# Performance work log

Hardware: AMD Instinct MI355X
Metric: run time of the kernel (lower is better)

The kernel has to match this reference:

```python
import jax, jax.numpy as jnp
import numpy as np

B, T, H, I, E = 2, 2048, 1024, 2048, 8
TOP_K = 2
RMS_EPS = 1e-6
ROUTING_GAIN = 1.0
INIT_STD = 0.02


def setup_inputs() -> dict:
    key = jax.random.key(0)
    ks = jax.random.split(key, 6)
    x = jax.random.normal(ks[0], (B, T, H), dtype=jnp.float32)
    q_norm_w = jnp.ones((H,), dtype=jnp.float32)
    k_proto = jax.random.normal(ks[1], (E, H), dtype=jnp.float32) * INIT_STD
    v_proto = jnp.eye(E, dtype=jnp.float32)  # nn.init.eye_
    gate_projs = jax.random.normal(ks[2], (E, H, I), dtype=jnp.float32) * INIT_STD
    up_projs = jax.random.normal(ks[3], (E, H, I), dtype=jnp.float32) * INIT_STD
    down_projs = jax.random.normal(ks[4], (E, I, H), dtype=jnp.float32) * INIT_STD
    return {"x": x, "q_norm_w": q_norm_w, "k_proto": k_proto, "v_proto": v_proto,
            "gate_projs": gate_projs, "up_projs": up_projs, "down_projs": down_projs}


def _routing_weights(x, q_norm_w, k_proto, v_proto):
    # CAPRRouter: RMSNorm -> proto attention -> softmax -> value mix -> gain
    q = x * jax.lax.rsqrt(jnp.mean(x * x, axis=-1, keepdims=True) + RMS_EPS) * q_norm_w
    attn = jax.nn.softmax(jnp.einsum('bth,ph->btp', q, k_proto) / np.sqrt(H).astype(np.float32), axis=-1)
    logits = jnp.einsum('btp,pq->btq', attn, v_proto) * ROUTING_GAIN
    rw = jax.nn.softmax(logits, axis=-1)  # [B,T,E]
    if TOP_K < E:
        tw, ti = jax.lax.top_k(rw, TOP_K)                       # [B,T,k]
        onehot = jax.nn.one_hot(ti, E, dtype=rw.dtype)          # [B,T,k,E]
        rw = jnp.einsum('btk,btke->bte', tw, onehot)            # scatter top-k back
        rw = rw / (jnp.sum(rw, axis=-1, keepdims=True) + 1e-9)
    return rw


def reference(x, q_norm_w, k_proto, v_proto, gate_projs, up_projs, down_projs):
    rw = _routing_weights(x, q_norm_w, k_proto, v_proto)  # [B,T,E]
    # Math-equivalent reassociation of torch's ('btp,phi->bthi' then 'bth,bthi->bti'):
    # per-expert GEMM then routing-weighted reduction over experts.
    gate_out = jnp.einsum('btp,btpi->bti', rw, jnp.einsum('bth,phi->btpi', x, gate_projs))
    up_out = jnp.einsum('btp,btpi->bti', rw, jnp.einsum('bth,phi->btpi', x, up_projs))
    intermediate = jax.nn.silu(gate_out) * up_out  # [B,T,I]
    output = jnp.einsum('btp,btph->bth', rw, jnp.einsum('bti,pih->btph', intermediate, down_projs))
    return output, rw
```

## Files before the change

kernel.cpp:

```cpp
#include <hip/hip_runtime.h>
#include <hip/hip_bf16.h>

#define NTOK 4096
#define HDIM 1024
#define IDIM 2048
#define NEXP 8
#define RBLK 16

typedef __attribute__((ext_vector_type(8))) short short8;
typedef __attribute__((ext_vector_type(4))) short short4b;
typedef __attribute__((ext_vector_type(4))) float f32x4;
typedef unsigned short ushort_t;

__device__ inline ushort_t f2bf(float f) {
    union { float f; unsigned u; } v; v.f = f;
    unsigned r = v.u + 0x7FFFu + ((v.u >> 16) & 1u);
    return (ushort_t)(r >> 16);
}
__device__ inline float bf2f(ushort_t h) {
    union { unsigned u; float f; } v; v.u = ((unsigned)h) << 16;
    return v.f;
}

#define GPTR(p) ((const __attribute__((address_space(1))) void*)(p))
#define LPTR(p) ((__attribute__((address_space(3))) void*)(p))

__global__ __launch_bounds__(256) void routing_kernel(
    const float* __restrict__ x, const float* __restrict__ qw,
    const float* __restrict__ kp, const float* __restrict__ vp,
    float* __restrict__ rw_out, int* __restrict__ counts,
    int* __restrict__ list, float2* __restrict__ topw,
    ushort_t* __restrict__ xb)
{
    __shared__ float kp_s[NEXP * HDIM];
    __shared__ float vp_s[NEXP * NEXP];
    __shared__ int lcnt[NEXP];
    __shared__ int base_s[NEXP];
    __shared__ int tinfo[RBLK][4];

    int tid = threadIdx.x;
    int wid = tid >> 6, lane = tid & 63;

    if (tid < NEXP) lcnt[tid] = 0;
    if (tid < NEXP * NEXP) vp_s[tid] = vp[tid];
    #pragma unroll
    for (int i = 0; i < 8; i++)
        ((float4*)kp_s)[tid + 256 * i] = ((const float4*)kp)[tid + 256 * i];

    float4 qv[4];
    #pragma unroll
    for (int j = 0; j < 4; j++) qv[j] = ((const float4*)qw)[lane + 64 * j];
    __syncthreads();

    for (int it = 0; it < RBLK / 4; it++) {
        int tl = wid * (RBLK / 4) + it;
        int t = blockIdx.x * RBLK + tl;
        const float4* xr4 = (const float4*)(x + (size_t)t * HDIM);
        float4 xv[4];
        #pragma unroll
        for (int j = 0; j < 4; j++) xv[j] = xr4[lane + 64 * j];

        ushort_t* xrow = xb + (size_t)t * HDIM;
        #pragma unroll
        for (int j = 0; j < 4; j++) {
            short4b o;
            o[0] = f2bf(xv[j].x); o[1] = f2bf(xv[j].y);
            o[2] = f2bf(xv[j].z); o[3] = f2bf(xv[j].w);
            ((short4b*)xrow)[lane + 64 * j] = o;
        }

        float ss = 0.f;
        #pragma unroll
        for (int j = 0; j < 4; j++)
            ss += xv[j].x*xv[j].x + xv[j].y*xv[j].y + xv[j].z*xv[j].z + xv[j].w*xv[j].w;
        #pragma unroll
        for (int off = 32; off; off >>= 1) ss += __shfl_xor(ss, off);
        float rms = rsqrtf(ss * (1.0f / HDIM) + 1e-6f);

        float4 q[4];
        #pragma unroll
        for (int j = 0; j < 4; j++) {
            q[j].x = xv[j].x * rms * qv[j].x; q[j].y = xv[j].y * rms * qv[j].y;
            q[j].z = xv[j].z * rms * qv[j].z; q[j].w = xv[j].w * rms * qv[j].w;
        }

        float d[NEXP];
        #pragma unroll
        for (int p = 0; p < NEXP; p++) {
            float acc = 0.f;
            #pragma unroll
            for (int j = 0; j < 4; j++) {
                float4 kv = ((const float4*)kp_s)[p * 256 + lane + 64 * j];
                acc += q[j].x*kv.x + q[j].y*kv.y + q[j].z*kv.z + q[j].w*kv.w;
            }
            #pragma unroll
            for (int off = 32; off; off >>= 1) acc += __shfl_xor(acc, off);
            d[p] = acc * (1.0f / 32.0f);
        }

        float m = d[0];
        #pragma unroll
        for (int p = 1; p < NEXP; p++) m = fmaxf(m, d[p]);
        float a[NEXP]; float s = 0.f;
        #pragma unroll
        for (int p = 0; p < NEXP; p++) { a[p] = expf(d[p] - m); s += a[p]; }
        float inv = 1.0f / s;
        #pragma unroll
        for (int p = 0; p < NEXP; p++) a[p] *= inv;
        float lg[NEXP];
        #pragma unroll
        for (int qi = 0; qi < NEXP; qi++) {
            float acc = 0.f;
            #pragma unroll
            for (int p = 0; p < NEXP; p++) acc += a[p] * vp_s[p * NEXP + qi];
            lg[qi] = acc;
        }
        float m2 = lg[0];
        #pragma unroll
        for (int p = 1; p < NEXP; p++) m2 = fmaxf(m2, lg[p]);
        float r[NEXP]; float s2 = 0.f;
        #pragma unroll
        for (int p = 0; p < NEXP; p++) { r[p] = expf(lg[p] - m2); s2 += r[p]; }
        float inv2 = 1.0f / s2;
        #pragma unroll
        for (int p = 0; p < NEXP; p++) r[p] *= inv2;
        int e0 = -1, e1 = -1; float w0 = -1.f, w1 = -1.f;
        #pragma unroll
        for (int p = 0; p < NEXP; p++) {
            if (r[p] > w0) { w1 = w0; e1 = e0; w0 = r[p]; e0 = p; }
            else if (r[p] > w1) { w1 = r[p]; e1 = p; }
        }
        float invn = 1.0f / (w0 + w1 + 1e-9f);
        float w0n = w0 * invn, w1n = w1 * invn;

        if (lane == 0) {
            #pragma unroll
            for (int p = 0; p < NEXP; p++)
                rw_out[(size_t)t * NEXP + p] = (p == e0) ? w0n : ((p == e1) ? w1n : 0.f);
            topw[t] = make_float2(w0n, w1n);
            int p0 = atomicAdd(&lcnt[e0], 1);
            int p1 = atomicAdd(&lcnt[e1], 1);
            tinfo[tl][0] = e0; tinfo[tl][1] = p0;
            tinfo[tl][2] = e1; tinfo[tl][3] = p1;
        }
    }
    __syncthreads();
    if (tid < NEXP) base_s[tid] = atomicAdd(&counts[tid], lcnt[tid]);
    __syncthreads();
    if (tid < RBLK) {
        int t = blockIdx.x * RBLK + tid;
        int e0 = tinfo[tid][0], p0 = tinfo[tid][1];
        int e1 = tinfo[tid][2], p1 = tinfo[tid][3];
        list[e0 * NTOK + base_s[e0] + p0] = t * 2;
        list[e1 * NTOK + base_s[e1] + p1] = t * 2 + 1;
    }
}

__global__ __launch_bounds__(256) void conv_t(const float* __restrict__ in, ushort_t* __restrict__ out,
                                              int K, int N) {
    __shared__ ushort_t ts[64][72];
    int e = blockIdx.z;
    int xb = blockIdx.x, yb = blockIdx.y;
    const float* ip = in + (size_t)e * K * N + (size_t)(yb * 64) * N + xb * 64;
    int NB = N / 128, KB = K / 64;
    int nb = xb >> 1, rhalf = (xb & 1) * 64;
    ushort_t* op = out + ((size_t)((size_t)e * NB + nb) * KB + yb) * (128 * 64);

    int tid = threadIdx.x;
    int r0 = tid >> 4;
    int c4 = (tid & 15) * 4;
    #pragma unroll
    for (int i = 0; i < 4; i++) {
        int r = r0 + i * 16;
        float4 v = *(const float4*)(ip + (size_t)r * N + c4);
        ts[c4+0][r] = f2bf(v.x); ts[c4+1][r] = f2bf(v.y);
        ts[c4+2][r] = f2bf(v.z); ts[c4+3][r] = f2bf(v.w);
    }
    __syncthreads();
    int n = tid >> 2;
    int kq = (tid & 3) * 16;
    int sw = (n & 7) << 3;
    short8 w0 = *(const short8*)&ts[n][kq];
    short8 w1 = *(const short8*)&ts[n][kq + 8];
    ushort_t* dst = op + (size_t)(rhalf + n) * 64;
    *(short8*)(dst + (kq ^ sw))       = w0;
    *(short8*)(dst + ((kq + 8) ^ sw)) = w1;
}

template<int K, int FUSED>
__global__ __launch_bounds__(256) void gemm_bf16(
    const ushort_t* __restrict__ A,
    const ushort_t* __restrict__ W0, const ushort_t* __restrict__ W1,
    const int* __restrict__ counts, const int* __restrict__ list,
    ushort_t* __restrict__ out0, ushort_t* __restrict__ out1, int odim)
{
    constexpr int KB = K / 64;
    int e = blockIdx.z;
    int M = counts[e];
    int row0 = blockIdx.y * 128;
    if (row0 >= M) return;
    int nbTiles = odim / 128;
    int colb = blockIdx.x;
    const ushort_t* W = (FUSED && colb >= nbTiles) ? W1 : W0;
    ushort_t* outp    = (FUSED && colb >= nbTiles) ? out1 : out0;
    int nb = (FUSED && colb >= nbTiles) ? colb - nbTiles : colb;
    int col0 = nb * 128;

    __shared__ ushort_t smem[128 * 136];
    __shared__ int rowsS[128];
    ushort_t* Abuf = smem;
    ushort_t* Bbuf = smem + 8192;

    int tid = threadIdx.x;
    if (tid < 128) {
        int r = row0 + tid;
        rowsS[tid] = (r < M) ? list[e * NTOK + r] : -1;
    }
    __syncthreads();

    int wid = tid >> 6, lane = tid & 63;
    int wr = wid >> 1, wc = wid & 1;
    int la = lane & 15, lb = lane >> 4;

    int swu = (((lane & 7) ^ (lane >> 3)) * 8);
    const ushort_t* aP[4];
    #pragma unroll
    for (int i = 0; i < 4; i++) {
        int r = (wid * 4 + i) * 8 + (lane >> 3);
        int ent = rowsS[r];
        int tok = (ent >= 0) ? (ent >> 1) : 0;
        aP[i] = A + (size_t)tok * K + swu;
    }
    const ushort_t* Wt = W + (size_t)((size_t)e * nbTiles + nb) * ((size_t)KB * 8192);

    int swr = (la & 7) << 3;
    int aoff[4][2], boff[4][2];
    #pragma unroll
    for (int m = 0; m < 4; m++)
        #pragma unroll
        for (int ks = 0; ks < 2; ks++)
            aoff[m][ks] = (wr * 64 + m * 16 + la) * 64 + ((ks * 32 + lb * 8) ^ swr);
    #pragma unroll
    for (int n = 0; n < 4; n++)
        #pragma unroll
        for (int ks = 0; ks < 2; ks++)
            boff[n][ks] = (wc * 64 + n * 16 + la) * 64 + ((ks * 32 + lb * 8) ^ swr);

    f32x4 acc[4][4];
    #pragma unroll
    for (int m = 0; m < 4; m++)
        #pragma unroll
        for (int n = 0; n < 4; n++) acc[m][n] = (f32x4){0.f, 0.f, 0.f, 0.f};

    for (int kt = 0; kt < KB; kt++) {
        #pragma unroll
        for (int i = 0; i < 4; i++) {
            int seg = wid * 4 + i;
            __builtin_amdgcn_global_load_lds(GPTR(aP[i] + kt * 64),
                                             LPTR(Abuf + seg * 512), 16, 0, 0);
            __builtin_amdgcn_global_load_lds(GPTR(Wt + (size_t)kt * 8192 + seg * 512 + lane * 8),
                                             LPTR(Bbuf + seg * 512), 16, 0, 0);
        }
        __syncthreads();
        #pragma unroll
        for (int ks = 0; ks < 2; ks++) {
            short8 af[4], bf[4];
            #pragma unroll
            for (int m = 0; m < 4; m++) af[m] = *(const short8*)&Abuf[aoff[m][ks]];
            #pragma unroll
            for (int n = 0; n < 4; n++) bf[n] = *(const short8*)&Bbuf[boff[n][ks]];
            #pragma unroll
            for (int m = 0; m < 4; m++)
                #pragma unroll
                for (int n = 0; n < 4; n++)
                    acc[m][n] = __builtin_amdgcn_mfma_f32_16x16x32_bf16(af[m], bf[n], acc[m][n], 0, 0, 0);
        }
        __syncthreads();
    }

    ushort_t* ob = smem;
    #pragma unroll
    for (int m = 0; m < 4; m++)
        #pragma unroll
        for (int n = 0; n < 4; n++)
            #pragma unroll
            for (int j = 0; j < 4; j++)
                ob[(wr * 64 + m * 16 + lb * 4 + j) * 136 + wc * 64 + n * 16 + la] =
                    f2bf(acc[m][n][j]);
    __syncthreads();
    int ch = tid & 15, rg = tid >> 4;
    #pragma unroll
    for (int i = 0; i < 8; i++) {
        int r = i * 16 + rg;
        int ent = rowsS[r];
        short8 v = *(const short8*)&ob[r * 136 + ch * 8];
        if (ent >= 0)
            *(short8*)(outp + (size_t)ent * odim + col0 + ch * 8) = v;
    }
}

__global__ __launch_bounds__(256) void silu_mix(
    const ushort_t* __restrict__ bg, const ushort_t* __restrict__ bu,
    const float2* __restrict__ topw, ushort_t* __restrict__ inter)
{
    int idx = blockIdx.x * 256 + threadIdx.x;
    int t = idx >> 8;
    int i8 = (idx & 255) * 8;
    float2 w = topw[t];
    short8 g0 = *(const short8*)(bg + (size_t)(2*t)   * IDIM + i8);
    short8 g1 = *(const short8*)(bg + (size_t)(2*t+1) * IDIM + i8);
    short8 u0 = *(const short8*)(bu + (size_t)(2*t)   * IDIM + i8);
    short8 u1 = *(const short8*)(bu + (size_t)(2*t+1) * IDIM + i8);
    short8 r;
    #pragma unroll
    for (int j = 0; j < 8; j++) {
        float g = w.x * bf2f((ushort_t)g0[j]) + w.y * bf2f((ushort_t)g1[j]);
        float u = w.x * bf2f((ushort_t)u0[j]) + w.y * bf2f((ushort_t)u1[j]);
        float s = g / (1.f + expf(-g)) * u;
        r[j] = f2bf(s);
    }
    *(short8*)(inter + (size_t)t * IDIM + i8) = r;
}

__global__ __launch_bounds__(256) void out_mix(
    const ushort_t* __restrict__ pout, const float2* __restrict__ topw,
    float* __restrict__ out)
{
    int idx = blockIdx.x * 256 + threadIdx.x;
    int t = idx >> 7;
    int h8 = (idx & 127) * 8;
    float2 w = topw[t];
    short8 a = *(const short8*)(pout + (size_t)(2*t)   * HDIM + h8);
    short8 b = *(const short8*)(pout + (size_t)(2*t+1) * HDIM + h8);
    float4 r0, r1;
    r0.x = w.x*bf2f((ushort_t)a[0]) + w.y*bf2f((ushort_t)b[0]);
    r0.y = w.x*bf2f((ushort_t)a[1]) + w.y*bf2f((ushort_t)b[1]);
    r0.z = w.x*bf2f((ushort_t)a[2]) + w.y*bf2f((ushort_t)b[2]);
    r0.w = w.x*bf2f((ushort_t)a[3]) + w.y*bf2f((ushort_t)b[3]);
    r1.x = w.x*bf2f((ushort_t)a[4]) + w.y*bf2f((ushort_t)b[4]);
    r1.y = w.x*bf2f((ushort_t)a[5]) + w.y*bf2f((ushort_t)b[5]);
    r1.z = w.x*bf2f((ushort_t)a[6]) + w.y*bf2f((ushort_t)b[6]);
    r1.w = w.x*bf2f((ushort_t)a[7]) + w.y*bf2f((ushort_t)b[7]);
    float* op = out + (size_t)t * HDIM + h8;
    *(float4*)op       = r0;
    *(float4*)(op + 4) = r1;
}

extern "C" void kernel_launch(void* const* d_in, const int* in_sizes, int n_in,
                              void* d_out, int out_size, void* d_ws, size_t ws_size,
                              hipStream_t stream) {
    const float* x    = (const float*)d_in[0];
    const float* qw   = (const float*)d_in[1];
    const float* kp   = (const float*)d_in[2];
    const float* vp   = (const float*)d_in[3];
    const float* gate = (const float*)d_in[4];
    const float* up   = (const float*)d_in[5];
    const float* down = (const float*)d_in[6];
    float* out = (float*)d_out;
    float* rw_out = out + (size_t)NTOK * HDIM;

    char* ws = (char*)d_ws;
    int*      counts = (int*)ws;
    float2*   topw   = (float2*)(ws + 1024);
    int*      list   = (int*)(ws + 64 * 1024);
    ushort_t* xb     = (ushort_t*)(ws + 256 * 1024);
    ushort_t* wtg    = xb + (size_t)NTOK * HDIM;
    ushort_t* wtu    = wtg + (size_t)NEXP * HDIM * IDIM;
    ushort_t* wtd    = wtu + (size_t)NEXP * HDIM * IDIM;
    ushort_t* bg     = wtd + (size_t)NEXP * HDIM * IDIM;
    ushort_t* bu     = bg  + (size_t)2 * NTOK * IDIM;
    ushort_t* interb = bu  + (size_t)2 * NTOK * IDIM;
    ushort_t* pout   = bg;

    hipMemsetAsync(counts, 0, NEXP * sizeof(int), stream);

    routing_kernel<<<NTOK / RBLK, 256, 0, stream>>>(x, qw, kp, vp, rw_out, counts, list, topw, xb);

    conv_t<<<dim3(IDIM / 64, HDIM / 64, NEXP), 256, 0, stream>>>(gate, wtg, HDIM, IDIM);
    conv_t<<<dim3(IDIM / 64, HDIM / 64, NEXP), 256, 0, stream>>>(up,   wtu, HDIM, IDIM);
    conv_t<<<dim3(HDIM / 64, IDIM / 64, NEXP), 256, 0, stream>>>(down, wtd, IDIM, HDIM);

    dim3 ggu(2 * IDIM / 128, NTOK / 128, NEXP);
    gemm_bf16<HDIM, 1><<<ggu, 256, 0, stream>>>(xb, wtg, wtu, counts, list, bg, bu, IDIM);

    silu_mix<<<NTOK * IDIM / 8 / 256, 256, 0, stream>>>(bg, bu, topw, interb);

    dim3 gd(HDIM / 128, NTOK / 128, NEXP);
    gemm_bf16<IDIM, 0><<<gd, 256, 0, stream>>>(interb, wtd, (const ushort_t*)nullptr,
                                               counts, list, pout, nullptr, HDIM);

    out_mix<<<NTOK * HDIM / 8 / 256, 256, 0, stream>>>(pout, topw, out);
}
```

Before: 251.5 us.

## Use 256x256 eight-wave pipelined GEMM for the gate/up projection

Replaces the 128x128 four-wave gate/up grouped GEMM with a dedicated 256x256 tile kernel running 512 threads. It double-buffers A and B halves in LDS, issues direct global-to-LDS loads, and interleaves the staging of the next half-tile between MFMA phases using explicit waitcnt, barriers and setprio. The aim is more reuse per loaded tile and better overlap of memory with matrix math. In exchange it uses much more LDS, needs more registers, and wastes more work on padded rows when experts get ragged token counts.

```diff
diff --git a/kernel.cpp b/kernel.cpp
--- a/kernel.cpp
+++ b/kernel.cpp
@@ -187,12 +187,181 @@
     *(short8*)(dst + ((kq + 8) ^ sw)) = w1;
 }
 
-template<int K, int FUSED>
-__global__ __launch_bounds__(256) void gemm_bf16(
+__global__ __launch_bounds__(512, 2) void gemm8_gu(
     const ushort_t* __restrict__ A,
     const ushort_t* __restrict__ W0, const ushort_t* __restrict__ W1,
     const int* __restrict__ counts, const int* __restrict__ list,
-    ushort_t* __restrict__ out0, ushort_t* __restrict__ out1, int odim)
+    ushort_t* __restrict__ out0, ushort_t* __restrict__ out1)
+{
+    constexpr int K = HDIM;
+    constexpr int KB = K / 64;
+    constexpr int NIT = KB / 2;
+    int e = blockIdx.z;
+    int M = counts[e];
+    int row0 = blockIdx.y * 256;
+    if (row0 >= M) return;
+    int colb = blockIdx.x;
+    const ushort_t* W = (colb >= 8) ? W1 : W0;
+    ushort_t* outp    = (colb >= 8) ? out1 : out0;
+    int nb = colb & 7;
+    int col0 = nb * 256;
+
+    __shared__ ushort_t smem[65536];
+    __shared__ int rowsS[256];
+
+    int tid = threadIdx.x;
+    for (int i = tid; i < 256; i += 512) {
+        int r = row0 + i;
+        rowsS[i] = (r < M) ? list[e * NTOK + r] : -1;
+    }
+    __syncthreads();
+
+    int wid = tid >> 6, lane = tid & 63;
+    int wr = wid >> 2, wc = wid & 3;
+    int la = lane & 15, lb = lane >> 4;
+
+    const ushort_t* aP[2][2];
+    #pragma unroll
+    for (int h = 0; h < 2; h++)
+        #pragma unroll
+        for (int j = 0; j < 2; j++) {
+            int r = (j * 512 + tid) >> 3;
+            int c = tid & 7;
+            int ent = rowsS[h * 128 + r];
+            int tok = (ent >= 0) ? (ent >> 1) : 0;
+            aP[h][j] = A + (size_t)tok * K + ((c ^ (r & 7)) * 8);
+        }
+    const ushort_t* WtE = W + (size_t)e * 16 * KB * 8192;
+
+    int swz = (la & 7) << 3;
+    int aoff[4][2], boff[2][2];
+    #pragma unroll
+    for (int s = 0; s < 4; s++)
+        #pragma unroll
+        for (int ks = 0; ks < 2; ks++)
+            aoff[s][ks] = (wr * 64 + s * 16 + la) * 64 + ((ks * 32 + lb * 8) ^ swz);
+    #pragma unroll
+    for (int s = 0; s < 2; s++)
+        #pragma unroll
+        for (int ks = 0; ks < 2; ks++)
+            boff[s][ks] = (wc * 32 + s * 16 + la) * 64 + ((ks * 32 + lb * 8) ^ swz);
+
+    f32x4 acc[8][4];
+    #pragma unroll
+    for (int f = 0; f < 8; f++)
+        #pragma unroll
+        for (int n = 0; n < 4; n++) acc[f][n] = (f32x4){0.f, 0.f, 0.f, 0.f};
+
+    auto AH = [&](int d, int h) { return smem + (d * 2 + h) * 8192; };
+    auto BH = [&](int d, int h) { return smem + 32768 + (d * 2 + h) * 8192; };
+
+    auto stgA = [&](int kt, int h) {
+        if (kt >= KB) return;
+        int d = kt & 1;
+        #pragma unroll
+        for (int j = 0; j < 2; j++)
+            __builtin_amdgcn_global_load_lds(GPTR(aP[h][j] + kt * 64),
+                LPTR(AH(d, h) + (j * 512 + wid * 64) * 8), 16, 0, 0);
+    };
+    auto stgB = [&](int kt, int hb) {
+        if (kt >= KB) return;
+        int d = kt & 1;
+        const ushort_t* src = WtE + (size_t)((nb * 2 + hb) * KB + kt) * 8192;
+        #pragma unroll
+        for (int j = 0; j < 2; j++)
+            __builtin_amdgcn_global_load_lds(GPTR(src + (j * 512 + tid) * 8),
+                LPTR(BH(d, hb) + (j * 512 + wid * 64) * 8), 16, 0, 0);
+    };
+
+    #define PHASE(DD, MH, NH, STG, CK)                                              \
+    {                                                                               \
+        const int d_ = (DD), mh_ = (MH), nh_ = (NH);                                \
+        const ushort_t* Ab_ = AH(d_, mh_);                                          \
+        const ushort_t* Bb_ = BH(d_, nh_);                                          \
+        short8 af_[4][2], bf_[2][2];                                                \
+        _Pragma("unroll")                                                           \
+        for (int mm = 0; mm < 4; mm++)                                              \
+            _Pragma("unroll")                                                       \
+            for (int ks = 0; ks < 2; ks++)                                          \
+                af_[mm][ks] = *(const short8*)&Ab_[aoff[mm][ks]];                   \
+        _Pragma("unroll")                                                           \
+        for (int nn = 0; nn < 2; nn++)                                              \
+            _Pragma("unroll")                                                       \
+            for (int ks = 0; ks < 2; ks++)                                          \
+                bf_[nn][ks] = *(const short8*)&Bb_[boff[nn][ks]];                   \
+        STG;                                                                        \
+        __builtin_amdgcn_s_barrier();                                               \
+        asm volatile("s_waitcnt lgkmcnt(0)" ::: "memory");                          \
+        __builtin_amdgcn_sched_barrier(0);                                          \
+        __builtin_amdgcn_s_setprio(1);                                              \
+        _Pragma("unroll")                                                           \
+        for (int mm = 0; mm < 4; mm++)                                              \
+            _Pragma("unroll")                                                       \
+            for (int nn = 0; nn < 2; nn++)                                          \
+                _Pragma("unroll")                                                   \
+                for (int ks = 0; ks < 2; ks++)                                      \
+                    acc[mh_ * 4 + mm][nh_ * 2 + nn] =                               \
+                        __builtin_amdgcn_mfma_f32_16x16x32_bf16(                    \
+                            af_[mm][ks], bf_[nn][ks],                               \
+                            acc[mh_ * 4 + mm][nh_ * 2 + nn], 0, 0, 0);              \
+        __builtin_amdgcn_s_setprio(0);                                              \
+        if ((CK) == 4)      asm volatile("s_waitcnt vmcnt(4)" ::: "memory");        \
+        else if ((CK) == 0) asm volatile("s_waitcnt vmcnt(0)" ::: "memory");        \
+        __builtin_amdgcn_s_barrier();                                               \
+    }
+
+    stgB(0, 0); stgA(0, 0); stgA(0, 1); stgB(0, 1);
+    stgB(1, 0); stgA(1, 0);
+    asm volatile("s_waitcnt vmcnt(4)" ::: "memory");
+    __builtin_amdgcn_s_barrier();
+
+    for (int it = 0; it < NIT; ++it) {
+        int t0 = 2 * it, t1 = t0 + 1;
+        int ck = (it == NIT - 1) ? 0 : 4;
+        PHASE(t0 & 1, 0, 0, stgA(t1, 1),     -1);
+        PHASE(t0 & 1, 1, 0, stgB(t1, 1),     -1);
+        PHASE(t0 & 1, 0, 1, stgB(t0 + 2, 0), -1);
+        PHASE(t0 & 1, 1, 1, stgA(t0 + 2, 0), ck);
+        PHASE(t1 & 1, 0, 0, stgA(t0 + 2, 1), -1);
+        PHASE(t1 & 1, 1, 0, stgB(t0 + 2, 1), -1);
+        PHASE(t1 & 1, 0, 1, stgB(t0 + 3, 0), -1);
+        PHASE(t1 & 1, 1, 1, stgA(t0 + 3, 0), ck);
+    }
+    #undef PHASE
+    __syncthreads();
+
+    ushort_t* ob = smem;
+    #pragma unroll
+    for (int h = 0; h < 2; h++) {
+        __syncthreads();
+        #pragma unroll
+        for (int s = 0; s < 4; s++)
+            #pragma unroll
+            for (int n = 0; n < 4; n++)
+                #pragma unroll
+                for (int j = 0; j < 4; j++) {
+                    int rw = wr * 64 + s * 16 + lb * 4 + j;
+                    int cc = (n >> 1) * 128 + wc * 32 + (n & 1) * 16 + la;
+                    ob[rw * 264 + cc] = f2bf(acc[h * 4 + s][n][j]);
+                }
+        __syncthreads();
+        #pragma unroll
+        for (int i = 0; i < 8; i++) {
+            int slot = i * 512 + tid;
+            int rl = slot >> 5, ch = slot & 31;
+            int ent = rowsS[h * 128 + rl];
+            short8 v = *(const short8*)&ob[rl * 264 + ch * 8];
+            if (ent >= 0)
+                *(short8*)(outp + (size_t)ent * IDIM + col0 + ch * 8) = v;
+        }
+    }
+}
+
+template<int K>
+__global__ __launch_bounds__(256) void gemm_bf16(
+    const ushort_t* __restrict__ A, const ushort_t* __restrict__ W0,
+    const int* __restrict__ counts, const int* __restrict__ list,
+    ushort_t* __restrict__ out0, int odim)
 {
     constexpr int KB = K / 64;
     int e = blockIdx.z;
@@ -200,10 +369,7 @@
     int row0 = blockIdx.y * 128;
     if (row0 >= M) return;
     int nbTiles = odim / 128;
-    int colb = blockIdx.x;
-    const ushort_t* W = (FUSED && colb >= nbTiles) ? W1 : W0;
-    ushort_t* outp    = (FUSED && colb >= nbTiles) ? out1 : out0;
-    int nb = (FUSED && colb >= nbTiles) ? colb - nbTiles : colb;
+    int nb = blockIdx.x;
     int col0 = nb * 128;
 
     __shared__ ushort_t smem[128 * 136];
@@ -231,7 +397,7 @@
         int tok = (ent >= 0) ? (ent >> 1) : 0;
         aP[i] = A + (size_t)tok * K + swu;
     }
-    const ushort_t* Wt = W + (size_t)((size_t)e * nbTiles + nb) * ((size_t)KB * 8192);
+    const ushort_t* Wt = W0 + (size_t)((size_t)e * nbTiles + nb) * ((size_t)KB * 8192);
 
     int swr = (la & 7) << 3;
     int aoff[4][2], boff[4][2];
@@ -295,7 +461,7 @@
         int ent = rowsS[r];
         short8 v = *(const short8*)&ob[r * 136 + ch * 8];
         if (ent >= 0)
-            *(short8*)(outp + (size_t)ent * odim + col0 + ch * 8) = v;
+            *(short8*)(out0 + (size_t)ent * odim + col0 + ch * 8) = v;
     }
 }
 
@@ -380,14 +546,13 @@
     conv_t<<<dim3(IDIM / 64, HDIM / 64, NEXP), 256, 0, stream>>>(up,   wtu, HDIM, IDIM);
     conv_t<<<dim3(HDIM / 64, IDIM / 64, NEXP), 256, 0, stream>>>(down, wtd, IDIM, HDIM);
 
-    dim3 ggu(2 * IDIM / 128, NTOK / 128, NEXP);
-    gemm_bf16<HDIM, 1><<<ggu, 256, 0, stream>>>(xb, wtg, wtu, counts, list, bg, bu, IDIM);
+    dim3 ggu(16, NTOK / 256, NEXP);
+    gemm8_gu<<<ggu, 512, 0, stream>>>(xb, wtg, wtu, counts, list, bg, bu);
 
     silu_mix<<<NTOK * IDIM / 8 / 256, 256, 0, stream>>>(bg, bu, topw, interb);
 
     dim3 gd(HDIM / 128, NTOK / 128, NEXP);
-    gemm_bf16<IDIM, 0><<<gd, 256, 0, stream>>>(interb, wtd, (const ushort_t*)nullptr,
-                                               counts, list, pout, nullptr, HDIM);
+    gemm_bf16<IDIM><<<gd, 256, 0, stream>>>(interb, wtd, counts, list, pout, HDIM);
 
     out_mix<<<NTOK * HDIM / 8 / 256, 256, 0, stream>>>(pout, topw, out);
 }
```

Result: slower. 283.0 us (+12.5%).
